# Performance work log

Measured on AMD Instinct MI355X. Metric: run time of the kernel, lower is better.

## Reference

```python
import jax, jax.numpy as jnp
import numpy as np
import math

HID = 2048; NH = 16; NKV = 4; NG = NH // NKV
LORA = 512; D_ROPE = 64; D_NOPE = 128; D_V = 128
D_QK = D_NOPE + D_ROPE  # 192
B, S = 2, 2048
ROPE_BASE = 10000.0


def setup_inputs() -> dict:
    key = jax.random.key(0)
    ks = jax.random.split(key, 5)
    s = lambda fan_in: 1.0 / math.sqrt(fan_in)
    return {
        "hidden_states": jax.random.normal(ks[0], (B, S, HID), jnp.float32),
        "Wqkv": jax.random.uniform(ks[1], (HID, NH * D_QK + LORA), jnp.float32, -s(HID), s(HID)),
        "Wk_up": jax.random.uniform(ks[2], (LORA, NKV * D_QK), jnp.float32, -s(LORA), s(LORA)),
        "Wv_up": jax.random.uniform(ks[3], (LORA, NKV * D_V), jnp.float32, -s(LORA), s(LORA)),
        "Wo": jax.random.uniform(ks[4], (NH * D_V, HID), jnp.float32, -s(NH * D_V), s(NH * D_V)),
    }


def _rope(x, seq_len):
    # x: [b, s, h, D_ROPE]; standard rotate-half RoPE
    inv_freq = 1.0 / (ROPE_BASE ** (jnp.arange(0, D_ROPE, 2, dtype=jnp.float32) / D_ROPE))
    t = jnp.arange(seq_len, dtype=jnp.float32)
    freqs = jnp.outer(t, inv_freq)                      # [s, D_ROPE/2]
    emb = jnp.concatenate([freqs, freqs], axis=-1)      # [s, D_ROPE]
    cos = jnp.cos(emb)[None, :, None, :].astype(x.dtype)
    sin = jnp.sin(emb)[None, :, None, :].astype(x.dtype)
    x1, x2 = jnp.split(x, 2, axis=-1)
    rot = jnp.concatenate([-x2, x1], axis=-1)
    return x * cos + rot * sin


def reference(hidden_states, Wqkv, Wk_up, Wv_up, Wo):
    b, s, _ = hidden_states.shape
    qkv = hidden_states @ Wqkv                              # [b,s,NH*D_QK+LORA]
    q, c_kv = jnp.split(qkv, [NH * D_QK], axis=-1)
    q = q.reshape(b, s, NH, D_QK)
    k = (c_kv @ Wk_up).reshape(b, s, NKV, D_QK)
    v = (c_kv @ Wv_up).reshape(b, s, NKV, D_V)
    q_nope, q_rope = jnp.split(q, [D_NOPE], axis=-1)
    k_nope, k_rope = jnp.split(k, [D_NOPE], axis=-1)
    q = jnp.concatenate([q_nope, _rope(q_rope, s)], axis=-1)   # [b,s,NH,D_QK]
    k = jnp.concatenate([k_nope, _rope(k_rope, s)], axis=-1)   # [b,s,NKV,D_QK]
    # GQA broadcast: repeat_interleave kv heads to NH
    k = jnp.repeat(k, NG, axis=2)
    v = jnp.repeat(v, NG, axis=2)
    scale = 1.0 / math.sqrt(D_QK)
    scores = jnp.einsum("bqhd,bkhd->bhqk", q, k) * scale
    causal = jnp.tril(jnp.ones((s, s), bool))
    scores = jnp.where(causal[None, None], scores, jnp.finfo(scores.dtype).min)
    probs = jax.nn.softmax(scores, axis=-1)
    out = jnp.einsum("bhqk,bkhd->bqhd", probs, v).reshape(b, s, NH * D_V)
    return out @ Wo
```

## Files before the change

### kernel.cpp

```cpp
#include <hip/hip_runtime.h>
#include <hip/hip_bf16.h>
#include <math.h>

#define HIDN  2048
#define NH    16
#define NKV   4
#define LORA  512
#define D_ROPE 64
#define D_NOPE 128
#define D_VV  128
#define D_QKD 192
#define BATCH 2
#define SEQ   2048
#define NTOK  (BATCH*SEQ)
#define QKV_W (NH*D_QKD + LORA)
#define KW    (NKV*D_QKD)
#define VW    (NKV*D_VV)
#define AW    (NH*D_VV)
#define QSCALE 0.07216878364870323f
#define LOG2E  1.4426950408889634f

typedef __attribute__((ext_vector_type(8))) __bf16 bf16x8;
typedef __attribute__((ext_vector_type(4))) float f32x4;

static __device__ __forceinline__ unsigned short f2bf(float f) {
    unsigned int u = __builtin_bit_cast(unsigned int, f);
    u += 0x7fffu + ((u >> 16) & 1u);
    return (unsigned short)(u >> 16);
}
static __device__ __forceinline__ float bf2f(unsigned short v) {
    unsigned int u = (unsigned int)v << 16;
    return __builtin_bit_cast(float, u);
}
static __device__ __forceinline__ unsigned int cvt_pk_bf16(float lo, float hi) {
    unsigned int r;
    asm("v_cvt_pk_bf16_f32 %0, %1, %2" : "=v"(r) : "v"(lo), "v"(hi));
    return r;
}
static __device__ __forceinline__ void gl2lds16(const unsigned short* g, unsigned short* l) {
    __builtin_amdgcn_global_load_lds(
        (const __attribute__((address_space(1))) unsigned int*)g,
        (__attribute__((address_space(3))) unsigned int*)l, 16, 0, 0);
}

__global__ __launch_bounds__(256) void transpose_w(
    const float* __restrict__ W, unsigned short* __restrict__ Wt,
    int K, int N, int scale_ncols, float scale)
{
    __shared__ float T[64][68];
    const int tid = threadIdx.x;
    const int k0 = blockIdx.y * 64, n0 = blockIdx.x * 64;
    const int rr = tid >> 4;
    const int c4 = (tid & 15) * 4;

#pragma unroll
    for (int i = 0; i < 4; ++i) {
        int r = rr + 16 * i;
        *(float4*)&T[r][c4] = *(const float4*)&W[(size_t)(k0 + r) * N + n0 + c4];
    }
    __syncthreads();
#pragma unroll
    for (int i = 0; i < 4; ++i) {
        int nr = rr + 16 * i;
        float sc = (n0 + nr < scale_ncols) ? scale : 1.0f;
        unsigned short tmp[4];
#pragma unroll
        for (int j = 0; j < 4; ++j) tmp[j] = f2bf(T[c4 + j][nr] * sc);
        unsigned int p0 = (unsigned int)tmp[0] | ((unsigned int)tmp[1] << 16);
        unsigned int p1 = (unsigned int)tmp[2] | ((unsigned int)tmp[3] << 16);
        *(uint2*)&Wt[(size_t)(n0 + nr) * K + k0 + c4] = make_uint2(p0, p1);
    }
}

__global__ __launch_bounds__(256) void cast_plain(const float* __restrict__ src,
                                                  unsigned short* __restrict__ dst)
{
    int idx = blockIdx.x * 256 + threadIdx.x;
    float4 v = *(const float4*)&src[(size_t)idx * 4];
    unsigned int p0 = (unsigned int)f2bf(v.x) | ((unsigned int)f2bf(v.y) << 16);
    unsigned int p1 = (unsigned int)f2bf(v.z) | ((unsigned int)f2bf(v.w) << 16);
    *(uint2*)&dst[(size_t)idx * 4] = make_uint2(p0, p1);
}

template<int OUT_MODE>
__global__ __launch_bounds__(256) void gemm_bt(
    const unsigned short* __restrict__ A,
    const unsigned short* __restrict__ Bt,
    void* __restrict__ C,
    int K, int lda, int ldb, int ldc)
{
    __shared__ __align__(16) unsigned short As[128 * 32];
    __shared__ __align__(16) unsigned short Bs[128 * 32];

    const int tid  = threadIdx.x;
    const int w    = tid >> 6;
    const int lane = tid & 63;
    const int quad = lane >> 4;
    const int l15  = lane & 15;
    const int brow = blockIdx.y * 128;
    const int bcol = blockIdx.x * 128;
    const int wr   = (w >> 1) * 64;
    const int wc   = (w & 1) * 64;

    const int srow = lane >> 2;
    const int sseg = (lane & 3) * 8;
    const int r0   = w * 32;

    f32x4 acc[4][4];
#pragma unroll
    for (int mt = 0; mt < 4; ++mt)
#pragma unroll
        for (int nt = 0; nt < 4; ++nt) acc[mt][nt] = (f32x4){0.f, 0.f, 0.f, 0.f};

    const unsigned short* Ab = A  + (size_t)(brow + r0 + srow) * lda + sseg;
    const unsigned short* Bb = Bt + (size_t)(bcol + r0 + srow) * ldb + sseg;

    for (int k0 = 0; k0 < K; k0 += 32) {
        __syncthreads();
        gl2lds16(Ab + k0,                     As + r0 * 32);
        gl2lds16(Ab + k0 + (size_t)16 * lda,  As + (r0 + 16) * 32);
        gl2lds16(Bb + k0,                     Bs + r0 * 32);
        gl2lds16(Bb + k0 + (size_t)16 * ldb,  Bs + (r0 + 16) * 32);
        __syncthreads();

        bf16x8 af[4], bfr[4];
#pragma unroll
        for (int mt = 0; mt < 4; ++mt)
            af[mt] = __builtin_bit_cast(bf16x8,
                *(const uint4*)(As + (wr + mt * 16 + l15) * 32 + quad * 8));
#pragma unroll
        for (int nt = 0; nt < 4; ++nt)
            bfr[nt] = __builtin_bit_cast(bf16x8,
                *(const uint4*)(Bs + (wc + nt * 16 + l15) * 32 + quad * 8));
#pragma unroll
        for (int mt = 0; mt < 4; ++mt)
#pragma unroll
            for (int nt = 0; nt < 4; ++nt)
                acc[mt][nt] = __builtin_amdgcn_mfma_f32_16x16x32_bf16(
                    af[mt], bfr[nt], acc[mt][nt], 0, 0, 0);
    }

    if (OUT_MODE == 2) {
#pragma unroll
        for (int mt = 0; mt < 4; ++mt) {
            int row0 = brow + wr + mt * 16 + quad * 4;
            int r5   = row0 & 31;
            int pos  = ((r5 & 15) >> 2) * 8 + ((r5 >> 4) << 2);
            int prow0 = (row0 & ~31) | pos;
#pragma unroll
            for (int nt = 0; nt < 4; ++nt) {
                int col = bcol + wc + nt * 16 + l15;
                unsigned int p0 = (unsigned int)f2bf(acc[mt][nt][0]) |
                                  ((unsigned int)f2bf(acc[mt][nt][1]) << 16);
                unsigned int p1 = (unsigned int)f2bf(acc[mt][nt][2]) |
                                  ((unsigned int)f2bf(acc[mt][nt][3]) << 16);
                *(uint2*)&((unsigned short*)C)[(size_t)col * ldc + prow0] = make_uint2(p0, p1);
            }
        }
    } else {
#pragma unroll
        for (int mt = 0; mt < 4; ++mt)
#pragma unroll
            for (int i = 0; i < 4; ++i) {
                size_t row = (size_t)(brow + wr + mt * 16 + quad * 4 + i);
#pragma unroll
                for (int nt = 0; nt < 4; ++nt) {
                    int col = bcol + wc + nt * 16 + l15;
                    ((unsigned short*)C)[row * ldc + col] = f2bf(acc[mt][nt][i]);
                }
            }
    }
}

template<int OUT_MODE, int BN>
__global__ __launch_bounds__(512, 2) void gemm8p(
    const unsigned short* __restrict__ A,
    const unsigned short* __restrict__ Bt,
    void* __restrict__ C,
    int K, int lda, int ldb, int ldc)
{
    constexpr int BNF    = BN / 64;
    constexpr int LB     = BN / 64;
    constexpr int NLOADS = 4 + LB;
    constexpr int ASLOT  = 256 * 64;
    constexpr int BSLOT  = BN * 64;
    constexpr int SLOT   = ASLOT + BSLOT;

    extern __shared__ __align__(16) unsigned short lds[];

    const int tid  = threadIdx.x;
    const int w    = tid >> 6;
    const int lane = tid & 63;
    const int quad = lane >> 4;
    const int l15  = lane & 15;
    const int wm   = w >> 2;
    const int wn   = w & 3;

    int fid = blockIdx.y * gridDim.x + blockIdx.x;
    int nwg = gridDim.x * gridDim.y;
    int cpx = nwg >> 3;
    int swz = (fid & 7) * cpx + (fid >> 3);
    int bx  = swz % gridDim.x;
    int by  = swz / gridDim.x;
    const int brow = by * 256;
    const int bcol = bx * BN;

    int aoff[4], boff[LB];
#pragma unroll
    for (int i = 0; i < 4; ++i) {
        int chunk = (w * 4 + i) * 64 + lane;
        int row = chunk >> 3, c = chunk & 7;
        aoff[i] = row * lda + (c ^ (row & 7)) * 8;
    }
#pragma unroll
    for (int i = 0; i < LB; ++i) {
        int chunk = (w * LB + i) * 64 + lane;
        int row = chunk >> 3, c = chunk & 7;
        boff[i] = row * ldb + (c ^ (row & 7)) * 8;
    }
    const unsigned short* Ab = A  + (size_t)brow * lda;
    const unsigned short* Bb = Bt + (size_t)bcol * ldb;

    f32x4 acc[8][BNF];
#pragma unroll
    for (int mf = 0; mf < 8; ++mf)
#pragma unroll
        for (int nf = 0; nf < BNF; ++nf) acc[mf][nf] = (f32x4){0.f, 0.f, 0.f, 0.f};

    const int NT = K >> 6;

    auto stage = [&](int slot, int k0) {
        unsigned short* As = lds + slot * SLOT;
        unsigned short* Bs = As + ASLOT;
#pragma unroll
        for (int i = 0; i < 4; ++i)
            gl2lds16(Ab + k0 + aoff[i], As + (w * 4 + i) * 512);
#pragma unroll
        for (int i = 0; i < LB; ++i)
            gl2lds16(Bb + k0 + boff[i], Bs + (w * LB + i) * 512);
    };

    stage(0, 0);
    stage(1, 64);
    if constexpr (NLOADS == 8) asm volatile("s_waitcnt vmcnt(8)" ::: "memory");
    else                       asm volatile("s_waitcnt vmcnt(6)" ::: "memory");
    __builtin_amdgcn_s_barrier();
    __builtin_amdgcn_sched_barrier(0);

#pragma unroll 1
    for (int t = 0; t < NT; ++t) {
        const unsigned short* As = lds + (t & 1) * SLOT;
        const unsigned short* Bs = As + ASLOT;
        bf16x8 bq[BNF][2];

#pragma unroll
        for (int ph = 0; ph < 4; ++ph) {
            if (ph == 0) {
#pragma unroll
                for (int nf = 0; nf < BNF; ++nf)
#pragma unroll
                    for (int kk = 0; kk < 2; ++kk) {
                        int r = wn * (BN / 4) + nf * 16 + l15;
                        bq[nf][kk] = __builtin_bit_cast(bf16x8,
                            *(const uint4*)(Bs + r * 64 + (((kk * 4 + quad) ^ (r & 7)) * 8)));
                    }
            }
            bf16x8 af[2][2];
#pragma unroll
            for (int m = 0; m < 2; ++m)
#pragma unroll
                for (int kk = 0; kk < 2; ++kk) {
                    int r = wm * 128 + (ph * 2 + m) * 16 + l15;
                    af[m][kk] = __builtin_bit_cast(bf16x8,
                        *(const uint4*)(As + r * 64 + (((kk * 4 + quad) ^ (r & 7)) * 8)));
                }
            __builtin_amdgcn_s_barrier();
            __builtin_amdgcn_s_setprio(1);
#pragma unroll
            for (int m = 0; m < 2; ++m)
#pragma unroll
                for (int nf = 0; nf < BNF; ++nf)
#pragma unroll
                    for (int kk = 0; kk < 2; ++kk)
                        acc[ph * 2 + m][nf] = __builtin_amdgcn_mfma_f32_16x16x32_bf16(
                            af[m][kk], bq[nf][kk], acc[ph * 2 + m][nf], 0, 0, 0);
            __builtin_amdgcn_s_setprio(0);
            __builtin_amdgcn_s_barrier();
        }

        if (t + 2 < NT) {
            stage(t & 1, (t + 2) * 64);
            if constexpr (NLOADS == 8) asm volatile("s_waitcnt vmcnt(8)" ::: "memory");
            else                       asm volatile("s_waitcnt vmcnt(6)" ::: "memory");
            __builtin_amdgcn_s_barrier();
            __builtin_amdgcn_sched_barrier(0);
        } else if (t + 1 < NT) {
            asm volatile("s_waitcnt vmcnt(0)" ::: "memory");
            __builtin_amdgcn_s_barrier();
            __builtin_amdgcn_sched_barrier(0);
        }
    }

#pragma unroll
    for (int mf = 0; mf < 8; ++mf) {
#pragma unroll
        for (int i = 0; i < 4; ++i) {
            size_t row = (size_t)(brow + wm * 128 + mf * 16 + quad * 4 + i);
#pragma unroll
            for (int nf = 0; nf < BNF; ++nf) {
                int col = bcol + wn * (BN / 4) + nf * 16 + l15;
                if (OUT_MODE == 1)
                    ((unsigned short*)C)[row * ldc + col] = f2bf(acc[mf][nf][i]);
                else
                    ((float*)C)[row * ldc + col] = acc[mf][nf][i];
            }
        }
    }
}

__global__ __launch_bounds__(256) void rope_bf16(unsigned short* __restrict__ qkvb,
                                                 unsigned short* __restrict__ kb)
{
    int idx = blockIdx.x * 256 + threadIdx.x;
    int i    = idx & 31;
    int head = (idx >> 5) % 20;
    int t    = idx / (20 * 32);
    if (t >= NTOK) return;
    int pos = t & (SEQ - 1);

    const float LOG_BASE_OVER_32 = 0.28782313662425572f;
    float ang = (float)pos * __expf(-(float)i * LOG_BASE_OVER_32);
    float c = cosf(ang);
    float sn = sinf(ang);

    unsigned short* p;
    if (head < NH) p = qkvb + (size_t)t * QKV_W + head * D_QKD + D_NOPE;
    else           p = kb   + (size_t)t * KW    + (head - NH) * D_QKD + D_NOPE;

    float x1 = bf2f(p[i]), x2 = bf2f(p[i + 32]);
    p[i]      = f2bf(x1 * c - x2 * sn);
    p[i + 32] = f2bf(x2 * c + x1 * sn);
}

__global__ __launch_bounds__(256) void attn_mfma(
    const unsigned short* __restrict__ qkvb,
    const unsigned short* __restrict__ kb,
    const unsigned short* __restrict__ vt,
    unsigned short* __restrict__ attnb)
{
    __shared__ __align__(16) unsigned short KsL[2 * 32 * 192];
    __shared__ __align__(16) unsigned short VtL[2 * 128 * 32];

    const int tid  = threadIdx.x;
    const int w    = tid >> 6;
    const int lane = tid & 63;
    const int quad = lane >> 4;
    const int l15  = lane & 15;

    const int bid = blockIdx.x;
    const int g   = bid >> 5;
    const int jj  = g & 7;
    const int m   = g >> 3;
    int qt;
    if      (m == 0) qt = 31 - jj;
    else if (m == 1) qt = 16 + jj;
    else if (m == 2) qt = 15 - jj;
    else             qt = jj;
    const int hb = bid & 31;
    const int h  = hb & 15;
    const int b  = hb >> 4;
    const int kvh = h >> 2;

    const int x7   = l15 & 7;
    const int vx   = (l15 >> 1) & 3;

    int koff[3], voff[2];
#pragma unroll
    for (int it = 0; it < 3; ++it) {
        int bidx = (w * 3 + it) * 64 + lane;
        int row  = bidx / 24;
        int sblk = bidx - row * 24;
        int gblk = sblk ^ (row & 7);
        koff[it] = row * KW + gblk * 8;
    }
#pragma unroll
    for (int it = 0; it < 2; ++it) {
        int bidx = (w * 2 + it) * 64 + lane;
        int row  = bidx >> 2;
        int gblk = (bidx & 3) ^ ((row >> 1) & 3);
        voff[it] = row * NTOK + gblk * 8;
    }
    const unsigned short* kp0 = kb + (size_t)(b * SEQ) * KW + kvh * D_QKD;
    const unsigned short* vp0 = vt + (size_t)(kvh * 128) * NTOK + b * SEQ;

    const int q0   = qt * 64;
    const int q0w  = q0 + w * 16;
    const int wmax = q0w + 15;

    bf16x8 qf[6];
    {
        const unsigned short* qp =
            qkvb + (size_t)(b * SEQ + q0w + l15) * QKV_W + h * D_QKD + quad * 8;
#pragma unroll
        for (int t = 0; t < 6; ++t)
            qf[t] = __builtin_bit_cast(bf16x8, *(const uint4*)(qp + t * 32));
    }

    f32x4 o[8];
#pragma unroll
    for (int c = 0; c < 8; ++c) o[c] = (f32x4){0.f, 0.f, 0.f, 0.f};
    float lp = 0.f;

    const int nt = 2 * qt + 2;

    {
#pragma unroll
        for (int it = 0; it < 3; ++it)
            gl2lds16(kp0 + koff[it], KsL + (w * 3 + it) * 512);
#pragma unroll
        for (int it = 0; it < 2; ++it)
            gl2lds16(vp0 + voff[it], VtL + (w * 2 + it) * 512);
    }
    __syncthreads();

    for (int tk = 0; tk < nt; ++tk) {
        const int k0  = tk * 32;
        const int cur = tk & 1;

        if (tk + 1 < nt) {
            const int nxt = cur ^ 1;
            const unsigned short* ks = kp0 + (size_t)(k0 + 32) * KW;
            const unsigned short* vs = vp0 + (k0 + 32);
#pragma unroll
            for (int it = 0; it < 3; ++it)
                gl2lds16(ks + koff[it], KsL + nxt * (32 * 192) + (w * 3 + it) * 512);
#pragma unroll
            for (int it = 0; it < 2; ++it)
                gl2lds16(vs + voff[it], VtL + nxt * (128 * 32) + (w * 2 + it) * 512);
        }

        if (k0 <= wmax) {
            const unsigned short* Kc = KsL + cur * (32 * 192);
            const unsigned short* Vc = VtL + cur * (128 * 32);

            f32x4 s[2];
            __builtin_amdgcn_s_setprio(1);
#pragma unroll
            for (int j = 0; j < 2; ++j) {
                f32x4 acc = {0.f, 0.f, 0.f, 0.f};
                const unsigned short* kr = Kc + (j * 16 + l15) * 192;
#pragma unroll
                for (int t = 0; t < 6; ++t) {
                    int sblk = (quad + 4 * t) ^ x7;
                    bf16x8 kf = __builtin_bit_cast(bf16x8, *(const uint4*)(kr + sblk * 8));
                    acc = __builtin_amdgcn_mfma_f32_16x16x32_bf16(kf, qf[t], acc, 0, 0, 0);
                }
                s[j] = acc;
            }
            __builtin_amdgcn_s_setprio(0);

            if (k0 + 31 <= q0w) {
#pragma unroll
                for (int j = 0; j < 2; ++j)
#pragma unroll
                    for (int i = 0; i < 4; ++i) {
                        float p = __builtin_amdgcn_exp2f(s[j][i]);
                        s[j][i] = p;
                        lp += p;
                    }
            } else {
                const int qrow = q0w + l15;
#pragma unroll
                for (int j = 0; j < 2; ++j)
#pragma unroll
                    for (int i = 0; i < 4; ++i) {
                        int kidx = k0 + j * 16 + quad * 4 + i;
                        float p = (kidx <= qrow) ? __builtin_amdgcn_exp2f(s[j][i]) : 0.f;
                        s[j][i] = p;
                        lp += p;
                    }
            }

            uint4 pk;
            pk.x = cvt_pk_bf16(s[0][0], s[0][1]);
            pk.y = cvt_pk_bf16(s[0][2], s[0][3]);
            pk.z = cvt_pk_bf16(s[1][0], s[1][1]);
            pk.w = cvt_pk_bf16(s[1][2], s[1][3]);
            bf16x8 pa = __builtin_bit_cast(bf16x8, pk);

            __builtin_amdgcn_s_setprio(1);
#pragma unroll
            for (int c = 0; c < 8; ++c) {
                bf16x8 vf = __builtin_bit_cast(bf16x8,
                    *(const uint4*)(Vc + (c * 16 + l15) * 32 + ((quad ^ vx) * 8)));
                o[c] = __builtin_amdgcn_mfma_f32_16x16x32_bf16(pa, vf, o[c], 0, 0, 0);
            }
            __builtin_amdgcn_s_setprio(0);
        }

        __syncthreads();
    }

    float lt = lp;
    lt += __shfl_xor(lt, 16);
    lt += __shfl_xor(lt, 32);

#pragma unroll
    for (int i = 0; i < 4; ++i) {
        float inv = 1.0f / __shfl(lt, (lane & 48) | (quad * 4 + i));
        size_t rowoff = (size_t)(b * SEQ + q0w + quad * 4 + i) * AW + h * D_VV + l15;
#pragma unroll
        for (int c = 0; c < 8; ++c)
            attnb[rowoff + c * 16] = f2bf(o[c][i] * inv);
    }
}

extern "C" void kernel_launch(void* const* d_in, const int* in_sizes, int n_in,
                              void* d_out, int out_size, void* d_ws, size_t ws_size,
                              hipStream_t stream)
{
    const float* X     = (const float*)d_in[0];
    const float* Wqkv  = (const float*)d_in[1];
    const float* Wk_up = (const float*)d_in[2];
    const float* Wv_up = (const float*)d_in[3];
    const float* Wo    = (const float*)d_in[4];
    float* out = (float*)d_out;

    unsigned short* Xb    = (unsigned short*)d_ws;
    unsigned short* Wqt   = Xb    + (size_t)NTOK * HIDN;
    unsigned short* Wkt   = Wqt   + (size_t)QKV_W * HIDN;
    unsigned short* Wvt   = Wkt   + (size_t)KW * LORA;
    unsigned short* Wot   = Wvt   + (size_t)VW * LORA;
    unsigned short* qkvb  = Wot   + (size_t)HIDN * AW;
    unsigned short* kb    = qkvb  + (size_t)NTOK * QKV_W;
    unsigned short* vtb   = kb    + (size_t)NTOK * KW;
    unsigned short* attnb = vtb   + (size_t)VW * NTOK;

    cast_plain<<<NTOK * HIDN / 4 / 256, 256, 0, stream>>>(X, Xb);
    transpose_w<<<dim3(QKV_W / 64, HIDN / 64), 256, 0, stream>>>(
        Wqkv, Wqt, HIDN, QKV_W, NH * D_QKD, QSCALE * LOG2E);
    transpose_w<<<dim3(KW / 64, LORA / 64), 256, 0, stream>>>(Wk_up, Wkt, LORA, KW, 0, 1.0f);
    transpose_w<<<dim3(VW / 64, LORA / 64), 256, 0, stream>>>(Wv_up, Wvt, LORA, VW, 0, 1.0f);
    transpose_w<<<dim3(AW / 64, HIDN / 64), 256, 0, stream>>>(Wo, Wot, HIDN, AW, 0, 1.0f);

    gemm8p<1, 256><<<dim3(QKV_W / 256, NTOK / 256), 512, 131072, stream>>>(
        Xb, Wqt, qkvb, HIDN, HIDN, HIDN, QKV_W);

    gemm_bt<1><<<dim3(KW / 128, NTOK / 128), 256, 0, stream>>>(
        qkvb + NH * D_QKD, Wkt, kb, LORA, QKV_W, LORA, KW);
    gemm_bt<2><<<dim3(VW / 128, NTOK / 128), 256, 0, stream>>>(
        qkvb + NH * D_QKD, Wvt, vtb, LORA, QKV_W, LORA, NTOK);

    rope_bf16<<<(NTOK * 20 * 32 + 255) / 256, 256, 0, stream>>>(qkvb, kb);

    attn_mfma<<<dim3(1024), 256, 0, stream>>>(qkvb, kb, vtb, attnb);

    gemm8p<0, 128><<<dim3(HIDN / 128, NTOK / 256), 512, 98304, stream>>>(
        attnb, Wot, out, AW, AW, AW, HIDN);
}
```

Baseline: 349.7 us.

## Interleave global-to-LDS prefetch with MFMA phases in gemm8p main loop

Restructures the gemm8p K-loop so each of the four MFMA phases issues part of the next tiles' global-to-LDS loads. A-rows for tile t+1 go into the other slot, and B-halves for tile t+2 go into the current slot after its B fragments are read. Fine-grained vmcnt waits replace the bulk stage-then-wait at the end of each iteration. The goal is to hide load latency behind compute and avoid the serialized load burst. In exchange it adds wraparound (dummy) loads at the loop tail and relies on carefully chosen vmcnt counts for correctness.

Result: faster. 336.1 us (-3.9%).

```diff
diff --git a/kernel.cpp b/kernel.cpp
--- a/kernel.cpp
+++ b/kernel.cpp
@@ -179,12 +179,15 @@
     void* __restrict__ C,
     int K, int lda, int ldb, int ldc)
 {
-    constexpr int BNF    = BN / 64;
-    constexpr int LB     = BN / 64;
-    constexpr int NLOADS = 4 + LB;
-    constexpr int ASLOT  = 256 * 64;
-    constexpr int BSLOT  = BN * 64;
-    constexpr int SLOT   = ASLOT + BSLOT;
+    constexpr int BNF = BN / 64;
+    constexpr int LB  = BN / 64;
+    constexpr int HB  = LB / 2;
+    constexpr int ASLOT = 256 * 64;
+    constexpr int BSLOT = BN * 64;
+    constexpr int SLOT  = ASLOT + BSLOT;
+    constexpr int V0 = 2;
+    constexpr int V1 = (LB == 4) ? 4 : 3;
+    constexpr int V3 = (LB == 4) ? 4 : 3;
 
     extern __shared__ __align__(16) unsigned short lds[];
 
@@ -205,22 +208,20 @@
     const int brow = by * 256;
     const int bcol = bx * BN;
 
-    int aoff[4], boff[LB];
-#pragma unroll
-    for (int i = 0; i < 4; ++i) {
-        int chunk = (w * 4 + i) * 64 + lane;
-        int row = chunk >> 3, c = chunk & 7;
-        aoff[i] = row * lda + (c ^ (row & 7)) * 8;
-    }
-#pragma unroll
-    for (int i = 0; i < LB; ++i) {
-        int chunk = (w * LB + i) * 64 + lane;
-        int row = chunk >> 3, c = chunk & 7;
-        boff[i] = row * ldb + (c ^ (row & 7)) * 8;
-    }
     const unsigned short* Ab = A  + (size_t)brow * lda;
     const unsigned short* Bb = Bt + (size_t)bcol * ldb;
 
+    const int lr   = lane >> 3;
+    const int lswz = ((lane & 7) ^ lr) * 8;
+    const int arow0 = (w < 4) ? (w * 8) : (128 + (w - 4) * 8);
+    const int asrc  = (arow0 + lr) * lda + lswz;
+    int brow0[HB], bsrc[HB];
+#pragma unroll
+    for (int c = 0; c < HB; ++c) {
+        brow0[c] = (w * HB + c) * 8;
+        bsrc[c]  = (brow0[c] + lr) * ldb + lswz;
+    }
+
     f32x4 acc[8][BNF];
 #pragma unroll
     for (int mf = 0; mf < 8; ++mf)
@@ -229,77 +230,137 @@
 
     const int NT = K >> 6;
 
-    auto stage = [&](int slot, int k0) {
-        unsigned short* As = lds + slot * SLOT;
-        unsigned short* Bs = As + ASLOT;
-#pragma unroll
-        for (int i = 0; i < 4; ++i)
-            gl2lds16(Ab + k0 + aoff[i], As + (w * 4 + i) * 512);
-#pragma unroll
-        for (int i = 0; i < LB; ++i)
-            gl2lds16(Bb + k0 + boff[i], Bs + (w * LB + i) * 512);
+    auto stageA = [&](int s, int tt, int p) {
+        gl2lds16(Ab + tt * 64 + p * 32 * lda + asrc,
+                 lds + s * SLOT + (arow0 + p * 32) * 64);
     };
-
-    stage(0, 0);
-    stage(1, 64);
-    if constexpr (NLOADS == 8) asm volatile("s_waitcnt vmcnt(8)" ::: "memory");
-    else                       asm volatile("s_waitcnt vmcnt(6)" ::: "memory");
+    auto stageB = [&](int s, int tt, int h) {
+#pragma unroll
+        for (int c = 0; c < HB; ++c)
+            gl2lds16(Bb + tt * 64 + h * (BN / 2) * ldb + bsrc[c],
+                     lds + s * SLOT + ASLOT + (brow0[c] + h * (BN / 2)) * 64);
+    };
+
+#pragma unroll
+    for (int p = 0; p < 4; ++p) stageA(0, 0, p);
+    stageB(0, 0, 0); stageB(0, 0, 1);
+    stageB(1, 1, 0); stageB(1, 1, 1);
+    asm volatile("s_waitcnt vmcnt(%0)" :: "i"(LB) : "memory");
     __builtin_amdgcn_s_barrier();
-    __builtin_amdgcn_sched_barrier(0);
 
 #pragma unroll 1
     for (int t = 0; t < NT; ++t) {
-        const unsigned short* As = lds + (t & 1) * SLOT;
+        const int s  = t & 1;
+        const int s1 = s ^ 1;
+        const int t1 = (t + 1 < NT) ? t + 1 : 0;
+        const int t2 = (t + 2 < NT) ? t + 2 : t + 2 - NT;
+        const unsigned short* As = lds + s * SLOT;
         const unsigned short* Bs = As + ASLOT;
-        bf16x8 bq[BNF][2];
-
-#pragma unroll
-        for (int ph = 0; ph < 4; ++ph) {
-            if (ph == 0) {
-#pragma unroll
-                for (int nf = 0; nf < BNF; ++nf)
-#pragma unroll
-                    for (int kk = 0; kk < 2; ++kk) {
-                        int r = wn * (BN / 4) + nf * 16 + l15;
-                        bq[nf][kk] = __builtin_bit_cast(bf16x8,
-                            *(const uint4*)(Bs + r * 64 + (((kk * 4 + quad) ^ (r & 7)) * 8)));
-                    }
-            }
-            bf16x8 af[2][2];
-#pragma unroll
-            for (int m = 0; m < 2; ++m)
-#pragma unroll
-                for (int kk = 0; kk < 2; ++kk) {
-                    int r = wm * 128 + (ph * 2 + m) * 16 + l15;
-                    af[m][kk] = __builtin_bit_cast(bf16x8,
-                        *(const uint4*)(As + r * 64 + (((kk * 4 + quad) ^ (r & 7)) * 8)));
-                }
-            __builtin_amdgcn_s_barrier();
-            __builtin_amdgcn_s_setprio(1);
-#pragma unroll
-            for (int m = 0; m < 2; ++m)
-#pragma unroll
-                for (int nf = 0; nf < BNF; ++nf)
-#pragma unroll
-                    for (int kk = 0; kk < 2; ++kk)
-                        acc[ph * 2 + m][nf] = __builtin_amdgcn_mfma_f32_16x16x32_bf16(
-                            af[m][kk], bq[nf][kk], acc[ph * 2 + m][nf], 0, 0, 0);
-            __builtin_amdgcn_s_setprio(0);
-            __builtin_amdgcn_s_barrier();
-        }
-
-        if (t + 2 < NT) {
-            stage(t & 1, (t + 2) * 64);
-            if constexpr (NLOADS == 8) asm volatile("s_waitcnt vmcnt(8)" ::: "memory");
-            else                       asm volatile("s_waitcnt vmcnt(6)" ::: "memory");
-            __builtin_amdgcn_s_barrier();
-            __builtin_amdgcn_sched_barrier(0);
-        } else if (t + 1 < NT) {
-            asm volatile("s_waitcnt vmcnt(0)" ::: "memory");
-            __builtin_amdgcn_s_barrier();
-            __builtin_amdgcn_sched_barrier(0);
-        }
-    }
+
+        bf16x8 bq[BNF][2], af[2][2];
+
+#pragma unroll
+        for (int nf = 0; nf < BNF; ++nf)
+#pragma unroll
+            for (int kk = 0; kk < 2; ++kk) {
+                int r = wn * (BN / 4) + nf * 16 + l15;
+                bq[nf][kk] = __builtin_bit_cast(bf16x8,
+                    *(const uint4*)(Bs + r * 64 + (((kk * 4 + quad) ^ (r & 7)) * 8)));
+            }
+#pragma unroll
+        for (int m = 0; m < 2; ++m)
+#pragma unroll
+            for (int kk = 0; kk < 2; ++kk) {
+                int r = wm * 128 + (0 * 2 + m) * 16 + l15;
+                af[m][kk] = __builtin_bit_cast(bf16x8,
+                    *(const uint4*)(As + r * 64 + (((kk * 4 + quad) ^ (r & 7)) * 8)));
+            }
+        stageA(s1, t1, 3);
+        __builtin_amdgcn_s_barrier();
+        __builtin_amdgcn_s_setprio(1);
+#pragma unroll
+        for (int m = 0; m < 2; ++m)
+#pragma unroll
+            for (int nf = 0; nf < BNF; ++nf)
+#pragma unroll
+                for (int kk = 0; kk < 2; ++kk)
+                    acc[0 + m][nf] = __builtin_amdgcn_mfma_f32_16x16x32_bf16(
+                        af[m][kk], bq[nf][kk], acc[0 + m][nf], 0, 0, 0);
+        __builtin_amdgcn_s_setprio(0);
+        asm volatile("s_waitcnt vmcnt(%0)" :: "i"(V0) : "memory");
+        __builtin_amdgcn_s_barrier();
+
+#pragma unroll
+        for (int m = 0; m < 2; ++m)
+#pragma unroll
+            for (int kk = 0; kk < 2; ++kk) {
+                int r = wm * 128 + (1 * 2 + m) * 16 + l15;
+                af[m][kk] = __builtin_bit_cast(bf16x8,
+                    *(const uint4*)(As + r * 64 + (((kk * 4 + quad) ^ (r & 7)) * 8)));
+            }
+        stageB(s, t2, 0);
+        stageA(s1, t1, 0);
+        __builtin_amdgcn_s_barrier();
+        __builtin_amdgcn_s_setprio(1);
+#pragma unroll
+        for (int m = 0; m < 2; ++m)
+#pragma unroll
+            for (int nf = 0; nf < BNF; ++nf)
+#pragma unroll
+                for (int kk = 0; kk < 2; ++kk)
+                    acc[2 + m][nf] = __builtin_amdgcn_mfma_f32_16x16x32_bf16(
+                        af[m][kk], bq[nf][kk], acc[2 + m][nf], 0, 0, 0);
+        __builtin_amdgcn_s_setprio(0);
+        asm volatile("s_waitcnt vmcnt(%0)" :: "i"(V1) : "memory");
+        __builtin_amdgcn_s_barrier();
+
+#pragma unroll
+        for (int m = 0; m < 2; ++m)
+#pragma unroll
+            for (int kk = 0; kk < 2; ++kk) {
+                int r = wm * 128 + (2 * 2 + m) * 16 + l15;
+                af[m][kk] = __builtin_bit_cast(bf16x8,
+                    *(const uint4*)(As + r * 64 + (((kk * 4 + quad) ^ (r & 7)) * 8)));
+            }
+        stageB(s, t2, 1);
+        stageA(s1, t1, 1);
+        __builtin_amdgcn_s_barrier();
+        __builtin_amdgcn_s_setprio(1);
+#pragma unroll
+        for (int m = 0; m < 2; ++m)
+#pragma unroll
+            for (int nf = 0; nf < BNF; ++nf)
+#pragma unroll
+                for (int kk = 0; kk < 2; ++kk)
+                    acc[4 + m][nf] = __builtin_amdgcn_mfma_f32_16x16x32_bf16(
+                        af[m][kk], bq[nf][kk], acc[4 + m][nf], 0, 0, 0);
+        __builtin_amdgcn_s_setprio(0);
+        __builtin_amdgcn_s_barrier();
+
+#pragma unroll
+        for (int m = 0; m < 2; ++m)
+#pragma unroll
+            for (int kk = 0; kk < 2; ++kk) {
+                int r = wm * 128 + (3 * 2 + m) * 16 + l15;
+                af[m][kk] = __builtin_bit_cast(bf16x8,
+                    *(const uint4*)(As + r * 64 + (((kk * 4 + quad) ^ (r & 7)) * 8)));
+            }
+        stageA(s1, t1, 2);
+        __builtin_amdgcn_s_barrier();
+        __builtin_amdgcn_s_setprio(1);
+#pragma unroll
+        for (int m = 0; m < 2; ++m)
+#pragma unroll
+            for (int nf = 0; nf < BNF; ++nf)
+#pragma unroll
+                for (int kk = 0; kk < 2; ++kk)
+                    acc[6 + m][nf] = __builtin_amdgcn_mfma_f32_16x16x32_bf16(
+                        af[m][kk], bq[nf][kk], acc[6 + m][nf], 0, 0, 0);
+        __builtin_amdgcn_s_setprio(0);
+        asm volatile("s_waitcnt vmcnt(%0)" :: "i"(V3) : "memory");
+        __builtin_amdgcn_s_barrier();
+    }
+    asm volatile("s_waitcnt vmcnt(0)" ::: "memory");
 
 #pragma unroll
     for (int mf = 0; mf < 8; ++mf) {
```

## Interleave global-to-LDS prefetch across MFMA phases in gemm8p main loop

Applied to the files above, without the earlier changes.

Restructures the gemm8p pipeline so that the A tile for the next k-step and the B tile for k+2 are issued in slices inside each of the four compute phases, rather than as one bulk stage after the compute loop. Each phase waits on a fixed vmcnt before its barrier, spreading memory traffic evenly and hiding load latency behind MFMA work. To keep the wait counts constant, the loop wraps around and issues redundant loads at the tail. This adds extra bandwidth in the last iterations and puts tighter ordering constraints on the A/B slot reuse across phases.

Measured after the change: 334.9 us. -4.2%, faster.

```diff
diff --git a/kernel.cpp b/kernel.cpp
--- a/kernel.cpp
+++ b/kernel.cpp
@@ -179,12 +179,13 @@
     void* __restrict__ C,
     int K, int lda, int ldb, int ldc)
 {
-    constexpr int BNF    = BN / 64;
-    constexpr int LB     = BN / 64;
-    constexpr int NLOADS = 4 + LB;
-    constexpr int ASLOT  = 256 * 64;
-    constexpr int BSLOT  = BN * 64;
-    constexpr int SLOT   = ASLOT + BSLOT;
+    constexpr int BNF = BN / 64;
+    constexpr int LB  = BN / 64;
+    constexpr int HB  = LB / 2;
+    constexpr int ASLOT = 256 * 64;
+    constexpr int BSLOT = BN * 64;
+    constexpr int SLOT  = ASLOT + BSLOT;
+    constexpr int NW  = 3 + 2 * HB;
 
     extern __shared__ __align__(16) unsigned short lds[];
 
@@ -205,22 +206,20 @@
     const int brow = by * 256;
     const int bcol = bx * BN;
 
-    int aoff[4], boff[LB];
-#pragma unroll
-    for (int i = 0; i < 4; ++i) {
-        int chunk = (w * 4 + i) * 64 + lane;
-        int row = chunk >> 3, c = chunk & 7;
-        aoff[i] = row * lda + (c ^ (row & 7)) * 8;
-    }
-#pragma unroll
-    for (int i = 0; i < LB; ++i) {
-        int chunk = (w * LB + i) * 64 + lane;
-        int row = chunk >> 3, c = chunk & 7;
-        boff[i] = row * ldb + (c ^ (row & 7)) * 8;
-    }
     const unsigned short* Ab = A  + (size_t)brow * lda;
     const unsigned short* Bb = Bt + (size_t)bcol * ldb;
 
+    const int lr   = lane >> 3;
+    const int lswz = ((lane & 7) ^ lr) * 8;
+    const int arow0 = (w < 4) ? (w * 8) : (128 + (w - 4) * 8);
+    const int asrc  = (arow0 + lr) * lda + lswz;
+    int brow0[HB], bsrc[HB];
+#pragma unroll
+    for (int c = 0; c < HB; ++c) {
+        brow0[c] = (w * HB + c) * 8;
+        bsrc[c]  = (brow0[c] + lr) * ldb + lswz;
+    }
+
     f32x4 acc[8][BNF];
 #pragma unroll
     for (int mf = 0; mf < 8; ++mf)
@@ -229,29 +228,35 @@
 
     const int NT = K >> 6;
 
-    auto stage = [&](int slot, int k0) {
-        unsigned short* As = lds + slot * SLOT;
-        unsigned short* Bs = As + ASLOT;
-#pragma unroll
-        for (int i = 0; i < 4; ++i)
-            gl2lds16(Ab + k0 + aoff[i], As + (w * 4 + i) * 512);
-#pragma unroll
-        for (int i = 0; i < LB; ++i)
-            gl2lds16(Bb + k0 + boff[i], Bs + (w * LB + i) * 512);
+    auto stageA = [&](int s, int tt, int p) {
+        gl2lds16(Ab + tt * 64 + p * 32 * lda + asrc,
+                 lds + s * SLOT + (arow0 + p * 32) * 64);
     };
-
-    stage(0, 0);
-    stage(1, 64);
-    if constexpr (NLOADS == 8) asm volatile("s_waitcnt vmcnt(8)" ::: "memory");
-    else                       asm volatile("s_waitcnt vmcnt(6)" ::: "memory");
+    auto stageB = [&](int s, int tt, int h) {
+#pragma unroll
+        for (int c = 0; c < HB; ++c)
+            gl2lds16(Bb + tt * 64 + h * (BN / 2) * ldb + bsrc[c],
+                     lds + s * SLOT + ASLOT + (brow0[c] + h * (BN / 2)) * 64);
+    };
+
+    stageB(0, 0, 0); stageB(0, 0, 1);
+    stageA(0, 0, 0); stageA(0, 0, 1); stageA(0, 0, 2);
+    stageB(1, 1, 0);
+    stageA(0, 0, 3);
+    stageB(1, 1, 1);
+    asm volatile("s_waitcnt vmcnt(%0)" :: "i"(NW) : "memory");
     __builtin_amdgcn_s_barrier();
-    __builtin_amdgcn_sched_barrier(0);
 
 #pragma unroll 1
     for (int t = 0; t < NT; ++t) {
-        const unsigned short* As = lds + (t & 1) * SLOT;
+        const int s  = t & 1;
+        const int s1 = s ^ 1;
+        const int t1 = (t + 1 < NT) ? t + 1 : 0;
+        const int t2 = (t + 2 < NT) ? t + 2 : t + 2 - NT;
+        const unsigned short* As = lds + s * SLOT;
         const unsigned short* Bs = As + ASLOT;
-        bf16x8 bq[BNF][2];
+
+        bf16x8 bq[BNF][2], af[2][2];
 
 #pragma unroll
         for (int ph = 0; ph < 4; ++ph) {
@@ -265,7 +270,6 @@
                             *(const uint4*)(Bs + r * 64 + (((kk * 4 + quad) ^ (r & 7)) * 8)));
                     }
             }
-            bf16x8 af[2][2];
 #pragma unroll
             for (int m = 0; m < 2; ++m)
 #pragma unroll
@@ -274,6 +278,9 @@
                     af[m][kk] = __builtin_bit_cast(bf16x8,
                         *(const uint4*)(As + r * 64 + (((kk * 4 + quad) ^ (r & 7)) * 8)));
                 }
+            stageA(s1, t1, ph);
+            if (ph == 2) stageB(s, t2, 0);
+            if (ph == 3) stageB(s, t2, 1);
             __builtin_amdgcn_s_barrier();
             __builtin_amdgcn_s_setprio(1);
 #pragma unroll
@@ -285,21 +292,11 @@
                         acc[ph * 2 + m][nf] = __builtin_amdgcn_mfma_f32_16x16x32_bf16(
                             af[m][kk], bq[nf][kk], acc[ph * 2 + m][nf], 0, 0, 0);
             __builtin_amdgcn_s_setprio(0);
+            asm volatile("s_waitcnt vmcnt(%0)" :: "i"(NW) : "memory");
             __builtin_amdgcn_s_barrier();
         }
-
-        if (t + 2 < NT) {
-            stage(t & 1, (t + 2) * 64);
-            if constexpr (NLOADS == 8) asm volatile("s_waitcnt vmcnt(8)" ::: "memory");
-            else                       asm volatile("s_waitcnt vmcnt(6)" ::: "memory");
-            __builtin_amdgcn_s_barrier();
-            __builtin_amdgcn_sched_barrier(0);
-        } else if (t + 1 < NT) {
-            asm volatile("s_waitcnt vmcnt(0)" ::: "memory");
-            __builtin_amdgcn_s_barrier();
-            __builtin_amdgcn_sched_barrier(0);
-        }
-    }
+    }
+    asm volatile("s_waitcnt vmcnt(0)" ::: "memory");
 
 #pragma unroll
     for (int mf = 0; mf < 8; ++mf) {
```
